# Kernel optimization log

Measured on AMD Instinct MI355X. Metric: run time of the kernel, lower is better.

## Reference

```python
import jax, jax.numpy as jnp
import numpy as np

B, C, D, H, W = 2, 128, 32, 64, 64  # ch_in=128, shurink=0 -> Cs = ch_out = C
Cs = C


def setup_inputs() -> dict:
    key = jax.random.key(0)
    ks = jax.random.split(key, 9)
    std = 1.0 / np.sqrt(C).astype(np.float32)
    x = jax.random.normal(ks[0], (B, C, D, H, W), jnp.float32)
    Wk = jax.random.normal(ks[1], (Cs, C), jnp.float32) * std
    bk = jax.random.normal(ks[2], (Cs,), jnp.float32) * std
    Wq = jax.random.normal(ks[3], (Cs, C), jnp.float32) * std
    bq = jax.random.normal(ks[4], (Cs,), jnp.float32) * std
    Wv = jax.random.normal(ks[5], (Cs, C), jnp.float32) * std
    bv = jax.random.normal(ks[6], (Cs,), jnp.float32) * std
    Wo = jax.random.normal(ks[7], (C, Cs), jnp.float32) * (1.0 / np.sqrt(Cs).astype(np.float32))
    bo = jax.random.normal(ks[8], (C,), jnp.float32) * std
    return {"x": x, "Wk": Wk, "bk": bk, "Wq": Wq, "bq": bq, "Wv": Wv, "bv": bv, "Wo": Wo, "bo": bo}


def reference(x, Wk, bk, Wq, bq, Wv, bv, Wo, bo):
    # 1x1x1 Conv3d == per-voxel linear over channels
    def proj(Wt, bt):
        return jnp.einsum('bcdhw,oc->bodhw', x, Wt) + bt[None, :, None, None, None]

    K = proj(Wk, bk)  # [B,Cs,D,H,W]
    Q = proj(Wq, bq)
    V = proj(Wv, bv)

    scale = 1.0 / jnp.sqrt(jnp.asarray(Cs, x.dtype))
    # per-pixel depth attention: scores[b,h,w,i,j] = sum_c K[b,c,i,h,w] * Q[b,c,j,h,w]
    scores = jnp.einsum('bcihw,bcjhw->bhwij', K, Q) * scale
    # torch softmax dim=1 on [N,D,D] == key-position axis i (axis=-2 here)
    A = jax.nn.softmax(scores, axis=-2)
    # a[b,c,j,h,w] = sum_i V[b,c,i,h,w] * A[b,h,w,i,j]  (== bmm(V, A))
    a = jnp.einsum('bcihw,bhwij->bcjhw', V, A)
    out = jnp.einsum('bcjhw,oc->bojhw', a, Wo) + bo[None, :, None, None, None]
    return x + out  # atten_factor = 1
```

## Files before the change

### kernel.cpp

```cpp
#include <hip/hip_runtime.h>

typedef _Float16 f16x8 __attribute__((ext_vector_type(8)));
typedef _Float16 f16x4 __attribute__((ext_vector_type(4)));
typedef float    f32x4 __attribute__((ext_vector_type(4)));

#define MFMA(a,b,c) __builtin_amdgcn_mfma_f32_16x16x32_f16((a),(b),(c),0,0,0)


__global__ __launch_bounds__(128) void prep_kernel(
    const float* __restrict__ Wk, const float* __restrict__ bk,
    const float* __restrict__ Wq, const float* __restrict__ bq,
    const float* __restrict__ Wv, const float* __restrict__ bv,
    const float* __restrict__ Wo, const float* __restrict__ bo,
    _Float16* __restrict__ wh, float* __restrict__ bf) {
  __shared__ float shK[128], shO[128];
  const int o = blockIdx.x;
  const int c = threadIdx.x;
  const float scale = 0.08838834764831844f;
  shK[c] = Wk[c*128 + o];
  shO[c] = Wo[o*128 + c];
  __syncthreads();
  float aM = 0.f, aV = 0.f, tK = 0.f, bV = 0.f;
  for (int m = 0; m < 128; ++m) {
    aM += shK[m] * Wq[m*128 + c];
    aV += shO[m] * Wv[m*128 + c];
    tK += shK[m] * bq[m];
    bV += shO[m] * bv[m];
  }
  wh[o*128 + c]         = (_Float16)(aM * scale);
  wh[16384 + o*128 + c] = (_Float16)aV;
  if (c == 0) { bf[o] = tK * scale; bf[128 + o] = bV + bo[o]; }
}

__device__ __forceinline__ f16x4 cvt4(f32x4 v, f32x4 b) {
  f16x4 r;
  r[0] = (_Float16)(v[0] + b[0]); r[1] = (_Float16)(v[1] + b[1]);
  r[2] = (_Float16)(v[2] + b[2]); r[3] = (_Float16)(v[3] + b[3]);
  return r;
}
__device__ __forceinline__ f16x4 cvt4z(f32x4 v) {
  f16x4 r;
  r[0] = (_Float16)v[0]; r[1] = (_Float16)v[1];
  r[2] = (_Float16)v[2]; r[3] = (_Float16)v[3];
  return r;
}

__device__ __forceinline__ int xsw(int row, int col ) {
  return ((row << 8) | (col << 1)) ^ (((row ^ (row >> 2)) & 7) << 4);
}

__global__ __launch_bounds__(1024, 8) void attn_kernel(
    const float* __restrict__ x, const _Float16* __restrict__ wh,
    const float* __restrict__ bfp, float* __restrict__ out) {
  __shared__ __align__(16) char lds[75776];
  char* XtB = lds;
  char* YtB = lds + 32768;
  _Float16* At = (_Float16*)(lds + 65536);

  const int tid  = threadIdx.x;
  const int lane = tid & 63;
  const int wv   = tid >> 6;
  const int quad = lane >> 4;
  const int l15  = lane & 15;

  const int bid = blockIdx.x;
  const int g = (bid & ~31) | ((bid & 7) << 2) | ((bid >> 3) & 3);
  const int b   = g >> 10;
  const int rem = g & 1023;
  const int h   = rem >> 4;
  const int wg  = rem & 15;
  const size_t pbase = (size_t)b * 16777216u + (size_t)(h*64 + wg*4);
  const f32x4 zz = {0.f, 0.f, 0.f, 0.f};

  const int mi = wv & 7, ni = wv >> 3;
  f16x8 wm[4];
#pragma unroll
  for (int kk = 0; kk < 4; ++kk)
    wm[kk] = *(const f16x8*)(wh + (mi*16 + l15)*128 + kk*32 + quad*8);
  const f32x4 t4 = *(const f32x4*)(bfp + mi*16 + quad*4);

  {
    const float* xg = x + pbase;
#pragma unroll
    for (int i = 0; i < 4; ++i) {
      const int idx = tid + i*1024;
      const int c = idx & 127, dd = idx >> 7;
      const f32x4 v = *(const f32x4*)(xg + (size_t)c*131072 + (size_t)dd*4096);
#pragma unroll
      for (int p = 0; p < 4; ++p)
        *(_Float16*)(XtB + xsw(dd*4 + p, c)) = (_Float16)v[p];
    }
  }
  __syncthreads();

  {
    f32x4 aY[4] = {zz, zz, zz, zz};
#pragma unroll
    for (int kk = 0; kk < 4; ++kk) {
      const int co = kk*32 + quad*8;
#pragma unroll
      for (int nt = 0; nt < 4; ++nt) {
        const f16x8 bfv = *(const f16x8*)(XtB + xsw(ni*64 + nt*16 + l15, co));
        aY[nt] = MFMA(wm[kk], bfv, aY[nt]);
      }
    }
#pragma unroll
    for (int nt = 0; nt < 4; ++nt)
      *(f16x4*)(YtB + xsw(ni*64 + nt*16 + l15, mi*16 + quad*4)) = cvt4(aY[nt], t4);
  }
  __syncthreads();

  if (wv < 4) {
    const int p = wv;
    f32x4 aS[2][2] = {{zz, zz}, {zz, zz}};
#pragma unroll
    for (int kk = 0; kk < 4; ++kk) {
      const int co = kk*32 + quad*8;
      f16x8 ak[2], by[2];
#pragma unroll
      for (int t = 0; t < 2; ++t) {
        ak[t] = *(const f16x8*)(XtB + xsw((t*16 + l15)*4 + p, co));
        by[t] = *(const f16x8*)(YtB + xsw((t*16 + l15)*4 + p, co));
      }
#pragma unroll
      for (int ti = 0; ti < 2; ++ti)
#pragma unroll
        for (int tj = 0; tj < 2; ++tj)
          aS[ti][tj] = MFMA(ak[ti], by[tj], aS[ti][tj]);
    }
#pragma unroll
    for (int tj = 0; tj < 2; ++tj) {
      float mx = aS[0][tj][0];
#pragma unroll
      for (int r = 1; r < 4; ++r) mx = fmaxf(mx, aS[0][tj][r]);
#pragma unroll
      for (int r = 0; r < 4; ++r) mx = fmaxf(mx, aS[1][tj][r]);
      mx = fmaxf(mx, __shfl_xor(mx, 16));
      mx = fmaxf(mx, __shfl_xor(mx, 32));
      float e[2][4];
      float den = 0.f;
#pragma unroll
      for (int ti = 0; ti < 2; ++ti)
#pragma unroll
        for (int r = 0; r < 4; ++r) { e[ti][r] = __expf(aS[ti][tj][r] - mx); den += e[ti][r]; }
      den += __shfl_xor(den, 16);
      den += __shfl_xor(den, 32);
      const float rr = 1.0f / den;
#pragma unroll
      for (int ti = 0; ti < 2; ++ti) {
        f16x4 av;
#pragma unroll
        for (int r = 0; r < 4; ++r) av[r] = (_Float16)(e[ti][r] * rr);
        *(f16x4*)(At + (p*32 + tj*16 + l15)*40 + ti*16 + quad*4) = av;
      }
    }
  }
  __syncthreads();

  f16x8 wp[4];
  {
#pragma unroll
    for (int kk = 0; kk < 4; ++kk)
      wp[kk] = *(const f16x8*)(wh + 16384 + ((wv & 7)*16 + l15)*128 + kk*32 + quad*8);
    const int p = wv & 3, mg = wv >> 2;
    f16x8 bA[2];
#pragma unroll
    for (int tj = 0; tj < 2; ++tj)
      bA[tj] = *(const f16x8*)(At + (p*32 + tj*16 + l15)*40 + quad*8);
#pragma unroll
    for (int t2 = 0; t2 < 2; ++t2) {
      const int ms = mg*2 + t2;
      f16x8 ax;
#pragma unroll
      for (int jj = 0; jj < 8; ++jj)
        ax[jj] = *(const _Float16*)(XtB + xsw((quad*8 + jj)*4 + p, ms*16 + l15));
#pragma unroll
      for (int tj = 0; tj < 2; ++tj) {
        const f32x4 aU = MFMA(ax, bA[tj], zz);
        *(f16x4*)(YtB + xsw((tj*16 + l15)*4 + p, ms*16 + quad*4)) = cvt4z(aU);
      }
    }
  }
  __syncthreads();

  {
    const int oi = wv & 7, mg6 = wv >> 3;
    f32x4 acc[4] = {zz, zz, zz, zz};
#pragma unroll
    for (int kk = 0; kk < 4; ++kk) {
      const int co = kk*32 + quad*8;
#pragma unroll
      for (int mt = 0; mt < 4; ++mt) {
        const f16x8 av = *(const f16x8*)(YtB + xsw((mg6*4 + mt)*16 + l15, co));
        acc[mt] = MFMA(av, wp[kk], acc[mt]);
      }
    }
    const int o = oi*16 + l15;
    const float bb = bfp[128 + o];
    float* outp = out + pbase + (size_t)o*131072;
#pragma unroll
    for (int mt = 0; mt < 4; ++mt) {
      const int colb = (mg6*4 + mt)*16 + quad*4;
      const int d = colb >> 2;
      f32x4 v;
#pragma unroll
      for (int r = 0; r < 4; ++r)
        v[r] = acc[mt][r] + bb +
               (float)*(const _Float16*)(XtB + xsw(colb + r, o));
      *(f32x4*)(outp + (size_t)d*4096) = v;
    }
  }
}

extern "C" void kernel_launch(void* const* d_in, const int* in_sizes, int n_in,
                              void* d_out, int out_size, void* d_ws, size_t ws_size,
                              hipStream_t stream) {
  const float* x  = (const float*)d_in[0];
  const float* Wk = (const float*)d_in[1];
  const float* bk = (const float*)d_in[2];
  const float* Wq = (const float*)d_in[3];
  const float* bq = (const float*)d_in[4];
  const float* Wv = (const float*)d_in[5];
  const float* bv = (const float*)d_in[6];
  const float* Wo = (const float*)d_in[7];
  const float* bo = (const float*)d_in[8];
  float* out = (float*)d_out;
  _Float16* wh = (_Float16*)d_ws;
  float* bf = (float*)((char*)d_ws + 65536);

  prep_kernel<<<dim3(128), dim3(128), 0, stream>>>(Wk, bk, Wq, bq, Wv, bv, Wo, bo, wh, bf);
  attn_kernel<<<dim3(2048), dim3(1024), 0, stream>>>(x, wh, bf, out);
}
```

Before: 386.4 us.

## Pre-transpose input to fp16 channel-contiguous layout in separate kernel

Adds a transpose kernel that converts x from fp32 NCDHW into an fp16 per-tile layout with channels contiguous, stored in workspace. The attention kernel then loads its tile with wide 16-byte vector reads instead of strided 16-byte fp32 gathers followed by scalar LDS stores. This trades an extra kernel launch and an extra global round trip (read fp32, write fp16, reread fp16) for better coalescing and cheaper LDS fills in the main kernel.

```diff
diff --git a/kernel.cpp b/kernel.cpp
--- a/kernel.cpp
+++ b/kernel.cpp
@@ -32,6 +32,35 @@
   if (c == 0) { bf[o] = tK * scale; bf[128 + o] = bV + bo[o]; }
 }
 
+__global__ __launch_bounds__(256) void transpose_kernel(
+    const float* __restrict__ x, _Float16* __restrict__ Xg) {
+  __shared__ _Float16 Lt[64 * 130];
+  const int bid = blockIdx.x;
+  const int h = bid & 63, d = (bid >> 6) & 31, b = bid >> 11;
+  const int tid = threadIdx.x;
+  const size_t rbase = (size_t)b*16777216u + (size_t)d*4096 + h*64;
+#pragma unroll
+  for (int i = 0; i < 8; ++i) {
+    const int chunk = tid + i*256;
+    const int c = chunk >> 4, wq = chunk & 15;
+    const f32x4 v = *(const f32x4*)(x + rbase + (size_t)c*131072 + wq*4);
+    Lt[(wq*4+0)*130 + c] = (_Float16)v[0];
+    Lt[(wq*4+1)*130 + c] = (_Float16)v[1];
+    Lt[(wq*4+2)*130 + c] = (_Float16)v[2];
+    Lt[(wq*4+3)*130 + c] = (_Float16)v[3];
+  }
+  __syncthreads();
+  const int gbase = b*1024 + h*16;
+#pragma unroll
+  for (int i = 0; i < 4; ++i) {
+    const int idx = tid + i*256;
+    const int w = idx >> 4, ck = (idx & 15) * 8;
+    const int wg = w >> 2, p = w & 3;
+    const f16x8 v = *(const f16x8*)(Lt + w*130 + ck);
+    *(f16x8*)(Xg + (size_t)(gbase + wg)*16384 + (d*4 + p)*128 + ck) = v;
+  }
+}
+
 __device__ __forceinline__ f16x4 cvt4(f32x4 v, f32x4 b) {
   f16x4 r;
   r[0] = (_Float16)(v[0] + b[0]); r[1] = (_Float16)(v[1] + b[1]);
@@ -50,7 +79,7 @@
 }
 
 __global__ __launch_bounds__(1024, 8) void attn_kernel(
-    const float* __restrict__ x, const _Float16* __restrict__ wh,
+    const _Float16* __restrict__ Xg, const _Float16* __restrict__ wh,
     const float* __restrict__ bfp, float* __restrict__ out) {
   __shared__ __align__(16) char lds[75776];
   char* XtB = lds;
@@ -80,15 +109,13 @@
   const f32x4 t4 = *(const f32x4*)(bfp + mi*16 + quad*4);
 
   {
-    const float* xg = x + pbase;
-#pragma unroll
-    for (int i = 0; i < 4; ++i) {
+    const _Float16* src = Xg + (size_t)g * 16384;
+#pragma unroll
+    for (int i = 0; i < 2; ++i) {
       const int idx = tid + i*1024;
-      const int c = idx & 127, dd = idx >> 7;
-      const f32x4 v = *(const f32x4*)(xg + (size_t)c*131072 + (size_t)dd*4096);
-#pragma unroll
-      for (int p = 0; p < 4; ++p)
-        *(_Float16*)(XtB + xsw(dd*4 + p, c)) = (_Float16)v[p];
+      const int row = idx >> 4, ck = (idx & 15) * 8;
+      const f16x8 v = *(const f16x8*)(src + row*128 + ck);
+      *(f16x8*)(XtB + xsw(row, ck)) = v;
     }
   }
   __syncthreads();
@@ -227,7 +254,9 @@
   float* out = (float*)d_out;
   _Float16* wh = (_Float16*)d_ws;
   float* bf = (float*)((char*)d_ws + 65536);
+  _Float16* Xg = (_Float16*)((char*)d_ws + 131072);
 
   prep_kernel<<<dim3(128), dim3(128), 0, stream>>>(Wk, bk, Wq, bq, Wv, bv, Wo, bo, wh, bf);
-  attn_kernel<<<dim3(2048), dim3(1024), 0, stream>>>(x, wh, bf, out);
-}
+  transpose_kernel<<<dim3(4096), dim3(256), 0, stream>>>(x, Xg);
+  attn_kernel<<<dim3(2048), dim3(1024), 0, stream>>>(Xg, wh, bf, out);
+}
```

Result: faster. 370.4 us (-4.1%).
